# Kernel optimization log

Measured on AMD Instinct MI355X. Metric: run time of the kernel, lower is better.

The kernel has to match this reference:

```python
import jax, jax.numpy as jnp
import numpy as np

B, T, V, E, H, K = 64, 1024, 50000, 128, 256, 20
HD = H // 2  # hidden per LSTM direction


def _p(key, i, shape, scale=0.05):
    return jax.random.normal(jax.random.fold_in(key, i), shape, dtype=jnp.float32) * scale


def setup_inputs():
    key = jax.random.key(0)
    k1, k2, k3 = jax.random.split(key, 3)
    lengths = jax.random.randint(k2, (B,), T // 4, T + 1)
    mask = jnp.arange(T)[None, :] < lengths[:, None]  # [B,T] bool, left-aligned
    x = jax.random.randint(k1, (B, T), 1, V)
    x = jnp.where(mask, x, 0).astype(jnp.int32)  # pad_idx = 0
    tags = jax.random.randint(k3, (B, T), 0, K).astype(jnp.int32)
    inp = {"x": x, "tags": tags, "mask": mask}
    pk = jax.random.key(1)
    inp["emb"] = _p(pk, 0, (V, E)).at[0].set(0.0)  # padding_idx row zeroed
    dims = [E, H]  # layer-1 input is concat of both directions = H
    i = 1
    for l in range(2):
        for suf in ["", "_rev"]:
            inp[f"w_ih_l{l}{suf}"] = _p(pk, i, (4 * HD, dims[l])); i += 1
            inp[f"w_hh_l{l}{suf}"] = _p(pk, i, (4 * HD, HD)); i += 1
            inp[f"b_ih_l{l}{suf}"] = _p(pk, i, (4 * HD,)); i += 1
            inp[f"b_hh_l{l}{suf}"] = _p(pk, i, (4 * HD,)); i += 1
    inp["ln_g"] = jnp.ones((H,), jnp.float32)
    inp["ln_b"] = jnp.zeros((H,), jnp.float32)
    inp["attn_w"] = _p(pk, i, (1, H)); i += 1
    inp["attn_b"] = _p(pk, i, (1,)); i += 1
    inp["fc1_w"] = _p(pk, i, (H, H)); i += 1
    inp["fc1_b"] = _p(pk, i, (H,)); i += 1
    inp["fc2_w"] = _p(pk, i, (K, H)); i += 1
    inp["fc2_b"] = _p(pk, i, (K,)); i += 1
    inp["crf_start"] = _p(pk, i, (K,)); i += 1
    inp["crf_end"] = _p(pk, i, (K,)); i += 1
    inp["crf_trans"] = _p(pk, i, (K, K)); i += 1
    return inp


def _lstm_dir(x, w_ih, w_hh, b_ih, b_hh, reverse):
    # x: [B,T,D] -> [B,T,HD]; torch gate order i,f,g,o
    xs = jnp.swapaxes(x, 0, 1)  # [T,B,D]
    pre = xs @ w_ih.T + b_ih + b_hh  # input contribution precomputed (GEMM)

    def step(carry, g_in):
        h, c = carry
        g = g_in + h @ w_hh.T
        i, f, gc, o = jnp.split(g, 4, axis=-1)
        c = jax.nn.sigmoid(f) * c + jax.nn.sigmoid(i) * jnp.tanh(gc)
        h = jax.nn.sigmoid(o) * jnp.tanh(c)
        return (h, c), h

    nB, nH = x.shape[0], w_hh.shape[1]
    init = (jnp.zeros((nB, nH), x.dtype), jnp.zeros((nB, nH), x.dtype))
    _, hs = jax.lax.scan(step, init, pre, reverse=reverse)
    return jnp.swapaxes(hs, 0, 1)


def _crf_nll(emissions, tags, mask, start, end, trans):
    # torchcrf: llh = score - logZ, reduction='sum'; module returns -llh.mean() (scalar)
    maskf = mask.astype(emissions.dtype)
    em_sc = jnp.take_along_axis(emissions, tags[..., None], axis=2)[..., 0]  # [B,T]
    tr_sc = trans[tags[:, :-1], tags[:, 1:]]  # [B,T-1]
    num = start[tags[:, 0]] + em_sc[:, 0] + jnp.sum(maskf[:, 1:] * (tr_sc + em_sc[:, 1:]), axis=1)
    last = jnp.sum(mask.astype(jnp.int32), axis=1) - 1
    last_tags = jnp.take_along_axis(tags, last[:, None], axis=1)[:, 0]
    num = num + end[last_tags]
    alpha0 = start[None, :] + emissions[:, 0]  # [B,K]
    em_t = jnp.swapaxes(emissions[:, 1:], 0, 1)  # [T-1,B,K]
    m_t = jnp.swapaxes(mask[:, 1:], 0, 1)  # [T-1,B]

    def step(alpha, inp):
        e, m = inp
        nxt = jax.scipy.special.logsumexp(alpha[:, :, None] + trans[None] + e[:, None, :], axis=1)
        return jnp.where(m[:, None], nxt, alpha), None

    alpha, _ = jax.lax.scan(step, alpha0, (em_t, m_t))
    logZ = jax.scipy.special.logsumexp(alpha + end[None, :], axis=1)
    return -jnp.sum(num - logZ)


def reference(x, tags, mask, emb,
              w_ih_l0, w_hh_l0, b_ih_l0, b_hh_l0,
              w_ih_l0_rev, w_hh_l0_rev, b_ih_l0_rev, b_hh_l0_rev,
              w_ih_l1, w_hh_l1, b_ih_l1, b_hh_l1,
              w_ih_l1_rev, w_hh_l1_rev, b_ih_l1_rev, b_hh_l1_rev,
              ln_g, ln_b, attn_w, attn_b, fc1_w, fc1_b, fc2_w, fc2_b,
              crf_start, crf_end, crf_trans):
    mask = mask.at[:, 0].set(True)
    h = emb[x]  # [B,T,E]
    # 2-layer bidirectional LSTM (eval mode: dropout = identity)
    h = jnp.concatenate([
        _lstm_dir(h, w_ih_l0, w_hh_l0, b_ih_l0, b_hh_l0, False),
        _lstm_dir(h, w_ih_l0_rev, w_hh_l0_rev, b_ih_l0_rev, b_hh_l0_rev, True)], axis=-1)
    h = jnp.concatenate([
        _lstm_dir(h, w_ih_l1, w_hh_l1, b_ih_l1, b_hh_l1, False),
        _lstm_dir(h, w_ih_l1_rev, w_hh_l1_rev, b_ih_l1_rev, b_hh_l1_rev, True)], axis=-1)
    # LayerNorm (eps=1e-5)
    mu = jnp.mean(h, axis=-1, keepdims=True)
    var = jnp.mean(jnp.square(h - mu), axis=-1, keepdims=True)
    h = (h - mu) * jax.lax.rsqrt(var + 1e-5) * ln_g + ln_b
    # masked attention + residual broadcast of context
    scores = (h @ attn_w.T)[..., 0] + attn_b[0]  # [B,T]
    scores = jnp.where(mask, scores, jnp.float32(-1e9))
    w = jax.nn.softmax(scores, axis=1)[..., None]  # [B,T,1]
    h = h + jnp.sum(h * w, axis=1, keepdims=True)
    # hidden_fc: Linear + ReLU (dropout identity in eval)
    h = jax.nn.relu(h @ fc1_w.T + fc1_b)
    emissions = h @ fc2_w.T + fc2_b  # [B,T,K]
    return _crf_nll(emissions, tags, mask, crf_start, crf_end, crf_trans)
```

## Files before the change

### kernel.cpp

```cpp
#include <hip/hip_runtime.h>
#include <stdint.h>

#define BB 64
#define TT 1024
#define EE 128

typedef __bf16 bf16x8 __attribute__((ext_vector_type(8)));
typedef float f32x4 __attribute__((ext_vector_type(4)));

#define MFMA16 __builtin_amdgcn_mfma_f32_16x16x32_bf16

__device__ __forceinline__ float bf2f(unsigned short u) {
  union { unsigned int i; float f; } v; v.i = ((unsigned int)u) << 16; return v.f;
}
__device__ __forceinline__ unsigned short f2bf(float f) {
  union { float f; unsigned int i; } v; v.f = f;
  return (unsigned short)((v.i + 0x7fffu + ((v.i >> 16) & 1u)) >> 16);
}
__device__ __forceinline__ float sigf(float x) {
  return __builtin_amdgcn_rcpf(1.f + __expf(-x));
}
__device__ __forceinline__ float tanhf_(float x) {
  return fmaf(2.f, __builtin_amdgcn_rcpf(1.f + __expf(-2.f * x)), -1.f);
}


__global__ __launch_bounds__(256) void cvtbf4(const float* __restrict__ s,
                                              unsigned short* __restrict__ d, int n4) {
  int i = blockIdx.x * 256 + threadIdx.x;
  if (i < n4) {
    float4 v = *(const float4*)&s[(size_t)i * 4];
    ushort4 o; o.x = f2bf(v.x); o.y = f2bf(v.y); o.z = f2bf(v.z); o.w = f2bf(v.w);
    *(ushort4*)&d[(size_t)i * 4] = o;
  }
}

__global__ __launch_bounds__(256) void bias_comb(const float* bi, const float* bh,
                                                 const float* bir, const float* bhr,
                                                 float* __restrict__ o) {
  int j = blockIdx.x * 256 + threadIdx.x;
  if (j < 1024) o[j] = (j < 512) ? (bi[j] + bh[j]) : (bir[j - 512] + bhr[j - 512]);
}

__global__ __launch_bounds__(256) void embed_k(const int* __restrict__ x,
                                               const float* __restrict__ emb,
                                               unsigned short* __restrict__ xe) {
  int i = blockIdx.x * 256 + threadIdx.x;
  int bt = i >> 5, e4 = (i & 31) << 2;
  float4 v = *(const float4*)&emb[(size_t)x[bt] * EE + e4];
  ushort4 o; o.x = f2bf(v.x); o.y = f2bf(v.y); o.z = f2bf(v.z); o.w = f2bf(v.w);
  *(ushort4*)&xe[(size_t)bt * EE + e4] = o;
}


template <bool RELU, bool REMAP>
__global__ __launch_bounds__(256) void gemm_bt(const unsigned short* __restrict__ A,
                                               const unsigned short* __restrict__ W,
                                               const float* __restrict__ bias,
                                               unsigned short* __restrict__ out,
                                               int M, int N, int K) {
  __shared__ unsigned short As[64][40];
  __shared__ unsigned short Ws[64][40];
  const int tid = threadIdx.x, wave = tid >> 6, lane = tid & 63;
  const int m0 = blockIdx.x * 64, n0 = blockIdx.y * 64;
  f32x4 acc[4] = {{0,0,0,0},{0,0,0,0},{0,0,0,0},{0,0,0,0}};
  const int r = tid >> 2, kc = (tid & 3) << 3;
  const int fr = lane & 15, kk = (lane >> 4) << 3;

  for (int k0 = 0; k0 < K; k0 += 32) {
    uint4 av = *(const uint4*)&A[(size_t)(m0 + r) * K + k0 + kc];
    uint4 wv = *(const uint4*)&W[(size_t)(n0 + r) * K + k0 + kc];
    *(uint4*)&As[r][kc] = av;
    *(uint4*)&Ws[r][kc] = wv;
    __syncthreads();
    bf16x8 af = *(const bf16x8*)&As[wave * 16 + fr][kk];
#pragma unroll
    for (int nt = 0; nt < 4; nt++) {
      bf16x8 bv = *(const bf16x8*)&Ws[nt * 16 + fr][kk];
      acc[nt] = MFMA16(af, bv, acc[nt], 0, 0, 0);
    }
    __syncthreads();
  }
  const int cr = (lane >> 4) << 2, cc = lane & 15;
#pragma unroll
  for (int nt = 0; nt < 4; nt++) {
    int gn = n0 + nt * 16 + cc;
    float bs = bias[gn];
#pragma unroll
    for (int rr = 0; rr < 4; rr++) {
      int gm = m0 + wave * 16 + cr + rr;
      float v = acc[nt][rr] + bs;
      if (RELU) v = fmaxf(v, 0.f);
      size_t off;
      if (REMAP) { int b = gm >> 10, t = gm & 1023; off = ((size_t)(t * 64 + b)) * N + gn; }
      else       { off = (size_t)gm * N + gn; }
      out[off] = f2bf(v);
    }
  }
}


__global__ __launch_bounds__(512) void lstm_scan8(const unsigned short* __restrict__ pre,
                                                  const unsigned short* __restrict__ whhb,
                                                  unsigned short* __restrict__ hout) {
  const int b = blockIdx.x, dir = blockIdx.y;
  const int tid = threadIdx.x;
  const int w = tid >> 6, lane = tid & 63;
  const int fr = lane & 15, q = lane >> 4;
  const int u = 16 * w + fr;
  const unsigned short* wb = whhb + (size_t)dir * 65536;

  bf16x8 af[4][4];
#pragma unroll
  for (int G = 0; G < 4; G++)
#pragma unroll
    for (int kt = 0; kt < 4; kt++)
      af[G][kt] = *(const bf16x8*)&wb[(size_t)(128 * G + 16 * w + fr) * 128 + kt * 32 + q * 8];
  asm volatile("" : "+v"(af[0][0]), "+v"(af[0][1]), "+v"(af[0][2]), "+v"(af[0][3]),
                    "+v"(af[1][0]), "+v"(af[1][1]), "+v"(af[1][2]), "+v"(af[1][3]),
                    "+v"(af[2][0]), "+v"(af[2][1]), "+v"(af[2][2]), "+v"(af[2][3]),
                    "+v"(af[3][0]), "+v"(af[3][1]), "+v"(af[3][2]), "+v"(af[3][3]));

  __shared__ alignas(16) unsigned short hS[2][128];
  if (tid < 128) { hS[0][tid] = 0; hS[1][tid] = 0; }

  const int t0 = dir ? 1023 : 0, st = dir ? -1 : 1;
  float c = 0.f;
  const unsigned short* pb = pre + (size_t)b * 1024 + dir * 512 + u;
  unsigned short* hob = hout + (size_t)b * 1024 * 256 + dir * 128 + u;

  unsigned short pg0, pg1, pg2, pg3;
  {
    size_t tb = (size_t)t0 * 65536;
    pg0 = pb[tb]; pg1 = pb[tb + 128]; pg2 = pb[tb + 256]; pg3 = pb[tb + 384];
  }
  __syncthreads();

  int p = 0;
  for (int s = 0; s < 1024; s++) {
    const int t = t0 + st * s;
    bf16x8 bv0 = *(const bf16x8*)&hS[p][q * 8];
    bf16x8 bv1 = *(const bf16x8*)&hS[p][32 + q * 8];
    bf16x8 bv2 = *(const bf16x8*)&hS[p][64 + q * 8];
    bf16x8 bv3 = *(const bf16x8*)&hS[p][96 + q * 8];
    f32x4 c0 = {0,0,0,0}, c1 = {0,0,0,0}, c2 = {0,0,0,0}, c3 = {0,0,0,0};
    c0 = MFMA16(bv0, af[0][0], c0, 0,0,0); c1 = MFMA16(bv0, af[1][0], c1, 0,0,0);
    c2 = MFMA16(bv0, af[2][0], c2, 0,0,0); c3 = MFMA16(bv0, af[3][0], c3, 0,0,0);
    c0 = MFMA16(bv1, af[0][1], c0, 0,0,0); c1 = MFMA16(bv1, af[1][1], c1, 0,0,0);
    c2 = MFMA16(bv1, af[2][1], c2, 0,0,0); c3 = MFMA16(bv1, af[3][1], c3, 0,0,0);
    c0 = MFMA16(bv2, af[0][2], c0, 0,0,0); c1 = MFMA16(bv2, af[1][2], c1, 0,0,0);
    c2 = MFMA16(bv2, af[2][2], c2, 0,0,0); c3 = MFMA16(bv2, af[3][2], c3, 0,0,0);
    c0 = MFMA16(bv3, af[0][3], c0, 0,0,0); c1 = MFMA16(bv3, af[1][3], c1, 0,0,0);
    c2 = MFMA16(bv3, af[2][3], c2, 0,0,0); c3 = MFMA16(bv3, af[3][3], c3, 0,0,0);

    unsigned short ng0 = 0, ng1 = 0, ng2 = 0, ng3 = 0;
    if (s + 1 < 1024) {
      size_t tb = (size_t)(t + st) * 65536;
      ng0 = pb[tb]; ng1 = pb[tb + 128]; ng2 = pb[tb + 256]; ng3 = pb[tb + 384];
    }

    float gi = c0[0] + bf2f(pg0);
    float gf = c1[0] + bf2f(pg1);
    float gg = c2[0] + bf2f(pg2);
    float go = c3[0] + bf2f(pg3);
    float cn = sigf(gf) * c + sigf(gi) * tanhf_(gg);
    c = cn;
    float h = sigf(go) * tanhf_(cn);
    pg0 = ng0; pg1 = ng1; pg2 = ng2; pg3 = ng3;
    unsigned short hb = f2bf(h);
    if (q == 0) {
      hS[p ^ 1][u] = hb;
      hob[(size_t)t * 256] = hb;
    }
    asm volatile("s_waitcnt lgkmcnt(0)\n\ts_barrier" ::: "memory");
    p ^= 1;
  }
}


__global__ __launch_bounds__(256) void ln_attn(const unsigned short* __restrict__ h,
                                               const float* __restrict__ g,
                                               const float* __restrict__ be,
                                               const float* __restrict__ aw,
                                               const float* __restrict__ ab,
                                               float* __restrict__ hln,
                                               float* __restrict__ sc) {
  int row = blockIdx.x * 4 + (threadIdx.x >> 6);
  int lane = threadIdx.x & 63;
  ushort4 u = *(const ushort4*)&h[(size_t)row * 256 + lane * 4];
  float vx = bf2f(u.x), vy = bf2f(u.y), vz = bf2f(u.z), vw = bf2f(u.w);
  float s = vx + vy + vz + vw;
#pragma unroll
  for (int o = 1; o < 64; o <<= 1) s += __shfl_xor(s, o);
  float mu = s * (1.f / 256.f);
  float dx = vx - mu, dy = vy - mu, dz = vz - mu, dw = vw - mu;
  float q = dx * dx + dy * dy + dz * dz + dw * dw;
#pragma unroll
  for (int o = 1; o < 64; o <<= 1) q += __shfl_xor(q, o);
  float inv = rsqrtf(q * (1.f / 256.f) + 1e-5f);
  float4 gg = *(const float4*)&g[lane * 4];
  float4 bb = *(const float4*)&be[lane * 4];
  float y0 = dx * inv * gg.x + bb.x;
  float y1 = dy * inv * gg.y + bb.y;
  float y2 = dz * inv * gg.z + bb.z;
  float y3 = dw * inv * gg.w + bb.w;
  float4 ov; ov.x = y0; ov.y = y1; ov.z = y2; ov.w = y3;
  *(float4*)&hln[(size_t)row * 256 + lane * 4] = ov;
  float4 av = *(const float4*)&aw[lane * 4];
  float p = y0 * av.x + y1 * av.y + y2 * av.z + y3 * av.w;
#pragma unroll
  for (int o = 1; o < 64; o <<= 1) p += __shfl_xor(p, o);
  if (lane == 0) sc[row] = p + ab[0];
}


__global__ __launch_bounds__(256) void attn_pool(const float* __restrict__ scores,
                                                 const int* __restrict__ x,
                                                 const float* __restrict__ h_ln,
                                                 float* __restrict__ pooled) {
  int b = blockIdx.x, tid = threadIdx.x;
  __shared__ float wls[1024];
  __shared__ float red[4];
  float mx = -1e30f;
  for (int t = tid; t < 1024; t += 256) {
    bool valid = (t == 0) || (x[b * 1024 + t] != 0);
    float s = valid ? scores[b * 1024 + t] : -1e9f;
    wls[t] = s;
    mx = fmaxf(mx, s);
  }
#pragma unroll
  for (int o = 1; o < 64; o <<= 1) mx = fmaxf(mx, __shfl_xor(mx, o));
  if ((tid & 63) == 0) red[tid >> 6] = mx;
  __syncthreads();
  mx = fmaxf(fmaxf(red[0], red[1]), fmaxf(red[2], red[3]));
  __syncthreads();
  float sm = 0.f;
  for (int t = tid; t < 1024; t += 256) {
    float e = __expf(wls[t] - mx);
    wls[t] = e;
    sm += e;
  }
#pragma unroll
  for (int o = 1; o < 64; o <<= 1) sm += __shfl_xor(sm, o);
  if ((tid & 63) == 0) red[tid >> 6] = sm;
  __syncthreads();
  sm = red[0] + red[1] + red[2] + red[3];
  float inv = 1.f / sm;
  float a0 = 0.f, a1 = 0.f, a2 = 0.f, a3 = 0.f;
  const float* hb = h_ln + (size_t)b * 1024 * 256 + tid;
  for (int t = 0; t < 1024; t += 4) {
    a0 = fmaf(wls[t + 0], hb[(size_t)(t + 0) * 256], a0);
    a1 = fmaf(wls[t + 1], hb[(size_t)(t + 1) * 256], a1);
    a2 = fmaf(wls[t + 2], hb[(size_t)(t + 2) * 256], a2);
    a3 = fmaf(wls[t + 3], hb[(size_t)(t + 3) * 256], a3);
  }
  pooled[b * 256 + tid] = ((a0 + a1) + (a2 + a3)) * inv;
}

__global__ __launch_bounds__(256) void h2add(const float* __restrict__ h_ln,
                                             const float* __restrict__ pooled,
                                             unsigned short* __restrict__ h2) {
  size_t i = ((size_t)blockIdx.x * 256 + threadIdx.x) * 4;
  int b = (int)(i >> 18);
  int cidx = (int)(i & 255);
  float4 v = *(const float4*)&h_ln[i];
  float4 p = *(const float4*)&pooled[b * 256 + cidx];
  ushort4 o;
  o.x = f2bf(v.x + p.x); o.y = f2bf(v.y + p.y);
  o.z = f2bf(v.z + p.z); o.w = f2bf(v.w + p.w);
  *(ushort4*)&h2[i] = o;
}


__global__ __launch_bounds__(256) void fc2_emis(const unsigned short* __restrict__ fin,
                                                const float* __restrict__ w,
                                                const float* __restrict__ bias,
                                                float* __restrict__ em) {
  int row = blockIdx.x * 4 + (threadIdx.x >> 6);
  int lane = threadIdx.x & 63;
  ushort4 u = *(const ushort4*)&fin[(size_t)row * 256 + lane * 4];
  float x0 = bf2f(u.x), x1 = bf2f(u.y), x2 = bf2f(u.z), x3 = bf2f(u.w);
  float acc[20];
#pragma unroll
  for (int jj = 0; jj < 20; jj++) {
    float4 wv = *(const float4*)&w[jj * 256 + lane * 4];
    acc[jj] = x0 * wv.x + x1 * wv.y + x2 * wv.z + x3 * wv.w;
  }
#pragma unroll
  for (int jj = 0; jj < 20; jj++) {
#pragma unroll
    for (int o = 1; o < 64; o <<= 1) acc[jj] += __shfl_xor(acc[jj], o);
  }
  if (lane == 0) {
#pragma unroll
    for (int jj = 0; jj < 20; jj++) em[(size_t)row * 20 + jj] = acc[jj] + bias[jj];
  }
}


__global__ __launch_bounds__(64) void crf_k(const float* __restrict__ em,
                                            const int* __restrict__ tags,
                                            const int* __restrict__ x,
                                            const float* __restrict__ cs,
                                            const float* __restrict__ ce,
                                            const float* __restrict__ ctr,
                                            float* __restrict__ part) {
  int b = blockIdx.x, lane = threadIdx.x;
  const float* eb = em + (size_t)b * 1024 * 20;
  const int* tb = tags + b * 1024;
  const int* xb = x + b * 1024;

  int cnt = 0;
  for (int t = lane; t < 1024; t += 64) cnt += (t == 0 || xb[t] != 0) ? 1 : 0;
#pragma unroll
  for (int o = 1; o < 64; o <<= 1) cnt += __shfl_xor(cnt, o);
  int len = cnt;

  float ns = 0.f;
  for (int t = 1 + lane; t < len; t += 64)
    ns += ctr[tb[t - 1] * 20 + tb[t]] + eb[(size_t)t * 20 + tb[t]];
#pragma unroll
  for (int o = 1; o < 64; o <<= 1) ns += __shfl_xor(ns, o);
  float num = ns + cs[tb[0]] + eb[tb[0]] + ce[tb[len - 1]];

  __shared__ float al[32];
  if (lane < 32) al[lane] = (lane < 20) ? (cs[lane] + eb[lane]) : -1e30f;
  __syncthreads();

  int p = lane / 20, jj = lane % 20;
  int i0 = p * 7;
  float trc[7];
#pragma unroll
  for (int i = 0; i < 7; i++)
    trc[i] = (i0 + i < 20) ? ctr[(i0 + i) * 20 + jj] : -1e30f;

  for (int t = 1; t < len; t++) {
    float aa[7];
    float m = -3e30f;
#pragma unroll
    for (int i = 0; i < 7; i++) {
      float a = ((i0 + i < 28) ? al[i0 + i] : -1e30f) + trc[i];
      aa[i] = a;
      m = fmaxf(m, a);
    }
    float m0 = __shfl(m, jj), m1 = __shfl(m, jj + 20), m2 = __shfl(m, jj + 40);
    float mj = fmaxf(fmaxf(m0, m1), m2);
    float s = 0.f;
#pragma unroll
    for (int i = 0; i < 7; i++) s += __expf(aa[i] - mj);
    float s0 = __shfl(s, jj), s1 = __shfl(s, jj + 20), s2 = __shfl(s, jj + 40);
    float na = mj + __logf(s0 + s1 + s2) + eb[(size_t)t * 20 + jj];
    __syncthreads();
    if (lane < 20) al[lane] = na;
    __syncthreads();
  }

  float v = (lane < 20) ? (al[lane] + ce[lane]) : -3e30f;
  float mm = v;
#pragma unroll
  for (int o = 1; o < 64; o <<= 1) mm = fmaxf(mm, __shfl_xor(mm, o));
  float ss = (lane < 20) ? __expf(v - mm) : 0.f;
#pragma unroll
  for (int o = 1; o < 64; o <<= 1) ss += __shfl_xor(ss, o);
  float logZ = mm + __logf(ss);
  if (lane == 0) part[b] = logZ - num;
}

__global__ __launch_bounds__(64) void finalsum(const float* __restrict__ part,
                                               float* __restrict__ out) {
  float v = part[threadIdx.x];
#pragma unroll
  for (int o = 1; o < 64; o <<= 1) v += __shfl_xor(v, o);
  if (threadIdx.x == 0) out[0] = v;
}


extern "C" void kernel_launch(void* const* d_in, const int* in_sizes, int n_in,
                              void* d_out, int out_size, void* d_ws, size_t ws_size,
                              hipStream_t stream) {
  (void)in_sizes; (void)n_in; (void)out_size; (void)ws_size;
  const int*   x     = (const int*)  d_in[0];
  const int*   tags  = (const int*)  d_in[1];
  const float* emb   = (const float*)d_in[3];
  const float* wih0  = (const float*)d_in[4];
  const float* whh0  = (const float*)d_in[5];
  const float* bih0  = (const float*)d_in[6];
  const float* bhh0  = (const float*)d_in[7];
  const float* wih0r = (const float*)d_in[8];
  const float* whh0r = (const float*)d_in[9];
  const float* bih0r = (const float*)d_in[10];
  const float* bhh0r = (const float*)d_in[11];
  const float* wih1  = (const float*)d_in[12];
  const float* whh1  = (const float*)d_in[13];
  const float* bih1  = (const float*)d_in[14];
  const float* bhh1  = (const float*)d_in[15];
  const float* wih1r = (const float*)d_in[16];
  const float* whh1r = (const float*)d_in[17];
  const float* bih1r = (const float*)d_in[18];
  const float* bhh1r = (const float*)d_in[19];
  const float* lng   = (const float*)d_in[20];
  const float* lnb   = (const float*)d_in[21];
  const float* attw  = (const float*)d_in[22];
  const float* attb  = (const float*)d_in[23];
  const float* fc1w  = (const float*)d_in[24];
  const float* fc1b  = (const float*)d_in[25];
  const float* fc2w  = (const float*)d_in[26];
  const float* fc2b  = (const float*)d_in[27];
  const float* cst   = (const float*)d_in[28];
  const float* cen   = (const float*)d_in[29];
  const float* ctr   = (const float*)d_in[30];

  char* base = (char*)d_ws;
  const size_t MB = 1024 * 1024;

  unsigned short* PRE  = (unsigned short*)(base);
  float*          HLN  = (float*)(base);
  unsigned short* H2   = (unsigned short*)(base + 64 * MB);
  unsigned short* FC1O = (unsigned short*)(base + 96 * MB);
  unsigned short* XEMB = (unsigned short*)(base + 128 * MB);
  unsigned short* HL0  = (unsigned short*)(base + 128 * MB);
  unsigned short* HL1  = (unsigned short*)(base + 128 * MB);
  float*          EM   = (float*)(base + 128 * MB);
  char* sm = base + 160 * MB;
  unsigned short* WIH0  = (unsigned short*)sm;  sm += (size_t)2 * 512 * 128 * 2;
  unsigned short* WIH1  = (unsigned short*)sm;  sm += (size_t)2 * 512 * 256 * 2;
  unsigned short* FC1W  = (unsigned short*)sm;  sm += (size_t)256 * 256 * 2;
  unsigned short* WHHB0 = (unsigned short*)sm;  sm += (size_t)2 * 512 * 128 * 2;
  unsigned short* WHHB1 = (unsigned short*)sm;  sm += (size_t)2 * 512 * 128 * 2;
  float* BIAS0 = (float*)sm; sm += 1024 * 4;
  float* BIAS1 = (float*)sm; sm += 1024 * 4;
  float* SCORE = (float*)sm; sm += (size_t)BB * TT * 4;
  float* POOL  = (float*)sm; sm += 64 * 256 * 4;
  float* PART  = (float*)sm; sm += 256;

  cvtbf4<<<64, 256, 0, stream>>>(wih0, WIH0, 65536 / 4);
  cvtbf4<<<64, 256, 0, stream>>>(wih0r, WIH0 + 65536, 65536 / 4);
  cvtbf4<<<128, 256, 0, stream>>>(wih1, WIH1, 131072 / 4);
  cvtbf4<<<128, 256, 0, stream>>>(wih1r, WIH1 + 131072, 131072 / 4);
  cvtbf4<<<64, 256, 0, stream>>>(fc1w, FC1W, 65536 / 4);
  cvtbf4<<<64, 256, 0, stream>>>(whh0, WHHB0, 65536 / 4);
  cvtbf4<<<64, 256, 0, stream>>>(whh0r, WHHB0 + 65536, 65536 / 4);
  cvtbf4<<<64, 256, 0, stream>>>(whh1, WHHB1, 65536 / 4);
  cvtbf4<<<64, 256, 0, stream>>>(whh1r, WHHB1 + 65536, 65536 / 4);
  bias_comb<<<4, 256, 0, stream>>>(bih0, bhh0, bih0r, bhh0r, BIAS0);
  bias_comb<<<4, 256, 0, stream>>>(bih1, bhh1, bih1r, bhh1r, BIAS1);

  embed_k<<<8192, 256, 0, stream>>>(x, emb, XEMB);

  gemm_bt<false, true><<<dim3(1024, 16), 256, 0, stream>>>(XEMB, WIH0, BIAS0, PRE, 65536, 1024, 128);
  lstm_scan8<<<dim3(64, 2), 512, 0, stream>>>(PRE, WHHB0, HL0);

  gemm_bt<false, true><<<dim3(1024, 16), 256, 0, stream>>>(HL0, WIH1, BIAS1, PRE, 65536, 1024, 256);
  lstm_scan8<<<dim3(64, 2), 512, 0, stream>>>(PRE, WHHB1, HL1);

  ln_attn<<<16384, 256, 0, stream>>>(HL1, lng, lnb, attw, attb, HLN, SCORE);
  attn_pool<<<64, 256, 0, stream>>>(SCORE, x, HLN, POOL);
  h2add<<<16384, 256, 0, stream>>>(HLN, POOL, H2);

  gemm_bt<true, false><<<dim3(1024, 4), 256, 0, stream>>>(H2, FC1W, fc1b, FC1O, 65536, 256, 256);
  fc2_emis<<<16384, 256, 0, stream>>>(FC1O, fc2w, fc2b, EM);

  crf_k<<<64, 64, 0, stream>>>(EM, tags, x, cst, cen, ctr, PART);
  finalsum<<<1, 64, 0, stream>>>(PART, (float*)d_out);
}
```

Baseline: 1.793 ms.

## Process two batch sequences per LSTM scan block to interleave independent recurrences

Each LSTM scan workgroup now advances two batch rows at once, sharing the register-resident recurrent weights and one barrier per timestep, and the grid is halved from 64 to 32 blocks per direction. The intent is to hide the serial MFMA and activation latency of one recurrence behind the independent work of the other, and to pay the per-step barrier cost once for two sequences. The cost is that only 64 workgroups are active, so fewer CUs are in use, and each step does twice the work on the serial path.

```diff
diff --git a/kernel.cpp b/kernel.cpp
--- a/kernel.cpp
+++ b/kernel.cpp
@@ -100,10 +100,10 @@
 }
 
 
-__global__ __launch_bounds__(512) void lstm_scan8(const unsigned short* __restrict__ pre,
+__global__ __launch_bounds__(512) void lstm_scan9(const unsigned short* __restrict__ pre,
                                                   const unsigned short* __restrict__ whhb,
                                                   unsigned short* __restrict__ hout) {
-  const int b = blockIdx.x, dir = blockIdx.y;
+  const int bA = blockIdx.x, bB = blockIdx.x + 32, dir = blockIdx.y;
   const int tid = threadIdx.x;
   const int w = tid >> 6, lane = tid & 63;
   const int fr = lane & 15, q = lane >> 4;
@@ -121,57 +121,92 @@
                     "+v"(af[2][0]), "+v"(af[2][1]), "+v"(af[2][2]), "+v"(af[2][3]),
                     "+v"(af[3][0]), "+v"(af[3][1]), "+v"(af[3][2]), "+v"(af[3][3]));
 
-  __shared__ alignas(16) unsigned short hS[2][128];
-  if (tid < 128) { hS[0][tid] = 0; hS[1][tid] = 0; }
+  __shared__ alignas(16) unsigned short hS[2][2][128];
+  if (tid < 128) { hS[0][0][tid] = 0; hS[0][1][tid] = 0; hS[1][0][tid] = 0; hS[1][1][tid] = 0; }
 
   const int t0 = dir ? 1023 : 0, st = dir ? -1 : 1;
-  float c = 0.f;
-  const unsigned short* pb = pre + (size_t)b * 1024 + dir * 512 + u;
-  unsigned short* hob = hout + (size_t)b * 1024 * 256 + dir * 128 + u;
-
-  unsigned short pg0, pg1, pg2, pg3;
+  float cA = 0.f, cB = 0.f;
+  const unsigned short* pbA = pre + (size_t)bA * 1024 + dir * 512 + u;
+  const unsigned short* pbB = pre + (size_t)bB * 1024 + dir * 512 + u;
+  unsigned short* hobA = hout + (size_t)bA * 1024 * 256 + dir * 128 + u;
+  unsigned short* hobB = hout + (size_t)bB * 1024 * 256 + dir * 128 + u;
+
+  unsigned short pgA0, pgA1, pgA2, pgA3, pgB0, pgB1, pgB2, pgB3;
   {
     size_t tb = (size_t)t0 * 65536;
-    pg0 = pb[tb]; pg1 = pb[tb + 128]; pg2 = pb[tb + 256]; pg3 = pb[tb + 384];
+    pgA0 = pbA[tb]; pgA1 = pbA[tb + 128]; pgA2 = pbA[tb + 256]; pgA3 = pbA[tb + 384];
+    pgB0 = pbB[tb]; pgB1 = pbB[tb + 128]; pgB2 = pbB[tb + 256]; pgB3 = pbB[tb + 384];
   }
   __syncthreads();
 
   int p = 0;
   for (int s = 0; s < 1024; s++) {
     const int t = t0 + st * s;
-    bf16x8 bv0 = *(const bf16x8*)&hS[p][q * 8];
-    bf16x8 bv1 = *(const bf16x8*)&hS[p][32 + q * 8];
-    bf16x8 bv2 = *(const bf16x8*)&hS[p][64 + q * 8];
-    bf16x8 bv3 = *(const bf16x8*)&hS[p][96 + q * 8];
-    f32x4 c0 = {0,0,0,0}, c1 = {0,0,0,0}, c2 = {0,0,0,0}, c3 = {0,0,0,0};
-    c0 = MFMA16(bv0, af[0][0], c0, 0,0,0); c1 = MFMA16(bv0, af[1][0], c1, 0,0,0);
-    c2 = MFMA16(bv0, af[2][0], c2, 0,0,0); c3 = MFMA16(bv0, af[3][0], c3, 0,0,0);
-    c0 = MFMA16(bv1, af[0][1], c0, 0,0,0); c1 = MFMA16(bv1, af[1][1], c1, 0,0,0);
-    c2 = MFMA16(bv1, af[2][1], c2, 0,0,0); c3 = MFMA16(bv1, af[3][1], c3, 0,0,0);
-    c0 = MFMA16(bv2, af[0][2], c0, 0,0,0); c1 = MFMA16(bv2, af[1][2], c1, 0,0,0);
-    c2 = MFMA16(bv2, af[2][2], c2, 0,0,0); c3 = MFMA16(bv2, af[3][2], c3, 0,0,0);
-    c0 = MFMA16(bv3, af[0][3], c0, 0,0,0); c1 = MFMA16(bv3, af[1][3], c1, 0,0,0);
-    c2 = MFMA16(bv3, af[2][3], c2, 0,0,0); c3 = MFMA16(bv3, af[3][3], c3, 0,0,0);
-
-    unsigned short ng0 = 0, ng1 = 0, ng2 = 0, ng3 = 0;
+    bf16x8 avA0 = *(const bf16x8*)&hS[0][p][q * 8];
+    bf16x8 avA1 = *(const bf16x8*)&hS[0][p][32 + q * 8];
+    bf16x8 avA2 = *(const bf16x8*)&hS[0][p][64 + q * 8];
+    bf16x8 avA3 = *(const bf16x8*)&hS[0][p][96 + q * 8];
+    f32x4 a0 = {0,0,0,0}, a1 = {0,0,0,0}, a2 = {0,0,0,0}, a3 = {0,0,0,0};
+    a0 = MFMA16(avA0, af[0][0], a0, 0,0,0); a1 = MFMA16(avA0, af[1][0], a1, 0,0,0);
+    a2 = MFMA16(avA0, af[2][0], a2, 0,0,0); a3 = MFMA16(avA0, af[3][0], a3, 0,0,0);
+    a0 = MFMA16(avA1, af[0][1], a0, 0,0,0); a1 = MFMA16(avA1, af[1][1], a1, 0,0,0);
+    a2 = MFMA16(avA1, af[2][1], a2, 0,0,0); a3 = MFMA16(avA1, af[3][1], a3, 0,0,0);
+    a0 = MFMA16(avA2, af[0][2], a0, 0,0,0); a1 = MFMA16(avA2, af[1][2], a1, 0,0,0);
+    a2 = MFMA16(avA2, af[2][2], a2, 0,0,0); a3 = MFMA16(avA2, af[3][2], a3, 0,0,0);
+    a0 = MFMA16(avA3, af[0][3], a0, 0,0,0); a1 = MFMA16(avA3, af[1][3], a1, 0,0,0);
+    a2 = MFMA16(avA3, af[2][3], a2, 0,0,0); a3 = MFMA16(avA3, af[3][3], a3, 0,0,0);
+    bf16x8 avB0 = *(const bf16x8*)&hS[1][p][q * 8];
+    bf16x8 avB1 = *(const bf16x8*)&hS[1][p][32 + q * 8];
+    bf16x8 avB2 = *(const bf16x8*)&hS[1][p][64 + q * 8];
+    bf16x8 avB3 = *(const bf16x8*)&hS[1][p][96 + q * 8];
+    f32x4 b0 = {0,0,0,0}, b1 = {0,0,0,0}, b2 = {0,0,0,0}, b3 = {0,0,0,0};
+    b0 = MFMA16(avB0, af[0][0], b0, 0,0,0); b1 = MFMA16(avB0, af[1][0], b1, 0,0,0);
+    b2 = MFMA16(avB0, af[2][0], b2, 0,0,0); b3 = MFMA16(avB0, af[3][0], b3, 0,0,0);
+    b0 = MFMA16(avB1, af[0][1], b0, 0,0,0); b1 = MFMA16(avB1, af[1][1], b1, 0,0,0);
+    b2 = MFMA16(avB1, af[2][1], b2, 0,0,0); b3 = MFMA16(avB1, af[3][1], b3, 0,0,0);
+    b0 = MFMA16(avB2, af[0][2], b0, 0,0,0); b1 = MFMA16(avB2, af[1][2], b1, 0,0,0);
+    b2 = MFMA16(avB2, af[2][2], b2, 0,0,0); b3 = MFMA16(avB2, af[3][2], b3, 0,0,0);
+    b0 = MFMA16(avB3, af[0][3], b0, 0,0,0); b1 = MFMA16(avB3, af[1][3], b1, 0,0,0);
+    b2 = MFMA16(avB3, af[2][3], b2, 0,0,0); b3 = MFMA16(avB3, af[3][3], b3, 0,0,0);
+
+    unsigned short nA0 = 0, nA1 = 0, nA2 = 0, nA3 = 0;
+    unsigned short nB0 = 0, nB1 = 0, nB2 = 0, nB3 = 0;
     if (s + 1 < 1024) {
       size_t tb = (size_t)(t + st) * 65536;
-      ng0 = pb[tb]; ng1 = pb[tb + 128]; ng2 = pb[tb + 256]; ng3 = pb[tb + 384];
+      nA0 = pbA[tb]; nA1 = pbA[tb + 128]; nA2 = pbA[tb + 256]; nA3 = pbA[tb + 384];
+      nB0 = pbB[tb]; nB1 = pbB[tb + 128]; nB2 = pbB[tb + 256]; nB3 = pbB[tb + 384];
     }
 
-    float gi = c0[0] + bf2f(pg0);
-    float gf = c1[0] + bf2f(pg1);
-    float gg = c2[0] + bf2f(pg2);
-    float go = c3[0] + bf2f(pg3);
-    float cn = sigf(gf) * c + sigf(gi) * tanhf_(gg);
-    c = cn;
-    float h = sigf(go) * tanhf_(cn);
-    pg0 = ng0; pg1 = ng1; pg2 = ng2; pg3 = ng3;
-    unsigned short hb = f2bf(h);
-    if (q == 0) {
-      hS[p ^ 1][u] = hb;
-      hob[(size_t)t * 256] = hb;
+    {
+      float gi = a0[0] + bf2f(pgA0);
+      float gf = a1[0] + bf2f(pgA1);
+      float gg = a2[0] + bf2f(pgA2);
+      float go = a3[0] + bf2f(pgA3);
+      float cn = sigf(gf) * cA + sigf(gi) * tanhf_(gg);
+      cA = cn;
+      float h = sigf(go) * tanhf_(cn);
+      unsigned short hb = f2bf(h);
+      if (q == 0) {
+        hS[0][p ^ 1][u] = hb;
+        hobA[(size_t)t * 256] = hb;
+      }
     }
+    {
+      float gi = b0[0] + bf2f(pgB0);
+      float gf = b1[0] + bf2f(pgB1);
+      float gg = b2[0] + bf2f(pgB2);
+      float go = b3[0] + bf2f(pgB3);
+      float cn = sigf(gf) * cB + sigf(gi) * tanhf_(gg);
+      cB = cn;
+      float h = sigf(go) * tanhf_(cn);
+      unsigned short hb = f2bf(h);
+      if (q == 0) {
+        hS[1][p ^ 1][u] = hb;
+        hobB[(size_t)t * 256] = hb;
+      }
+    }
+    pgA0 = nA0; pgA1 = nA1; pgA2 = nA2; pgA3 = nA3;
+    pgB0 = nB0; pgB1 = nB1; pgB2 = nB2; pgB3 = nB3;
     asm volatile("s_waitcnt lgkmcnt(0)\n\ts_barrier" ::: "memory");
     p ^= 1;
   }
@@ -448,10 +483,10 @@
   embed_k<<<8192, 256, 0, stream>>>(x, emb, XEMB);
 
   gemm_bt<false, true><<<dim3(1024, 16), 256, 0, stream>>>(XEMB, WIH0, BIAS0, PRE, 65536, 1024, 128);
-  lstm_scan8<<<dim3(64, 2), 512, 0, stream>>>(PRE, WHHB0, HL0);
+  lstm_scan9<<<dim3(32, 2), 512, 0, stream>>>(PRE, WHHB0, HL0);
 
   gemm_bt<false, true><<<dim3(1024, 16), 256, 0, stream>>>(HL0, WIH1, BIAS1, PRE, 65536, 1024, 256);
-  lstm_scan8<<<dim3(64, 2), 512, 0, stream>>>(PRE, WHHB1, HL1);
+  lstm_scan9<<<dim3(32, 2), 512, 0, stream>>>(PRE, WHHB1, HL1);
 
   ln_attn<<<16384, 256, 0, stream>>>(HL1, lng, lnb, attw, attb, HLN, SCORE);
   attn_pool<<<64, 256, 0, stream>>>(SCORE, x, HLN, POOL);
```

Measured after the change: 2.590 ms. +44.5%, slower.
